# Performance work log

Measured on AMD Instinct MI355X. Metric: run time of the kernel, lower is better.

The kernel has to match this reference:

```python
import jax, jax.numpy as jnp
import numpy as np

B, S, H = 16, 4096, 1024


def setup_inputs() -> dict:
    key = jax.random.key(0)
    ks = jax.random.split(key, 8)
    scale = 1.0 / np.sqrt(H)
    return {
        "s_t_hat": jax.random.normal(ks[0], (B, H), jnp.float32),
        "encoder_outputs": jax.random.normal(ks[1], (B, S, H), jnp.float32),
        "encoder_feature": jax.random.normal(ks[2], (B * S, H), jnp.float32),
        "enc_padding_mask": jnp.ones((B, S), jnp.float32),
        "coverage": jax.random.uniform(ks[3], (B, S), jnp.float32),
        # params: decode_proj (Linear H->H with bias), W_c (Linear 1->H, no bias,
        # stored as an [H] column), v (Linear H->1, no bias, stored as [H])
        "W_dec": jax.random.normal(ks[4], (H, H), jnp.float32) * scale,
        "b_dec": jnp.zeros((H,), jnp.float32),
        "W_c": jax.random.normal(ks[5], (H,), jnp.float32),
        "v": jax.random.normal(ks[6], (H,), jnp.float32) * scale,
    }


def reference(s_t_hat, encoder_outputs, encoder_feature, enc_padding_mask,
              coverage, W_dec, b_dec, W_c, v):
    b, s, h = encoder_outputs.shape
    # decode_proj: [B, H]
    dec_fea = s_t_hat @ W_dec.T + b_dec
    # broadcast add over seq + coverage feature (Linear(1->H) == outer product)
    att = (encoder_feature.reshape(b, s, h)
           + dec_fea[:, None, :]
           + coverage[:, :, None] * W_c[None, None, :])
    e = jnp.tanh(att)
    scores = jnp.einsum('bsh,h->bs', e, v)
    # masked softmax with renormalization (is_word=True path)
    attn = jax.nn.softmax(scores, axis=1) * enc_padding_mask
    attn = attn / (attn.sum(axis=1, keepdims=True) + 1e-20)
    # context vector: weighted sum of encoder outputs
    c_t = jnp.einsum('bs,bsh->bh', attn, encoder_outputs)
    return c_t, attn, attn, scores
```

## Files before the change

kernel.cpp:

```cpp
#include <hip/hip_runtime.h>

#define BB 16
#define SS 4096
#define HH 1024
#define SSPLIT 64

__device__ __forceinline__ float fast_tanh(float x) {
    x = fminf(fmaxf(x, -15.0f), 15.0f);
    float e = __expf(-2.0f * x);
    return (1.0f - e) * __builtin_amdgcn_rcpf(1.0f + e);
}

__device__ __forceinline__ float wave_reduce_sum(float v) {
#pragma unroll
    for (int off = 32; off > 0; off >>= 1) v += __shfl_xor(v, off, 64);
    return v;
}

__global__ __launch_bounds__(256) void dec_fea_kernel(
    const float* __restrict__ s_t_hat, const float* __restrict__ W_dec,
    const float* __restrict__ b_dec, float* __restrict__ dec_fea)
{
    int wave = (blockIdx.x * blockDim.x + threadIdx.x) >> 6;
    int lane = threadIdx.x & 63;
    int b = wave >> 10;
    int h = wave & (HH - 1);
    const float4* st4 = (const float4*)(s_t_hat + (size_t)b * HH);
    const float4* wd4 = (const float4*)(W_dec + (size_t)h * HH);
    float acc = 0.0f;
#pragma unroll
    for (int j = 0; j < 4; ++j) {
        int idx = lane + 64 * j;
        float4 a = st4[idx];
        float4 w = wd4[idx];
        acc += a.x * w.x + a.y * w.y + a.z * w.z + a.w * w.w;
    }
    acc = wave_reduce_sum(acc);
    if (lane == 0) dec_fea[wave] = acc + b_dec[h];
}

__global__ __launch_bounds__(256) void scores_kernel(
    const float* __restrict__ ef, const float* __restrict__ dec_fea,
    const float* __restrict__ cov, const float* __restrict__ W_c,
    const float* __restrict__ v, float* __restrict__ scores)
{
    int row = (blockIdx.x * blockDim.x + threadIdx.x) >> 6;
    int lane = threadIdx.x & 63;
    int b = row >> 12;
    float cv = cov[row];
    const float4* ef4 = (const float4*)(ef + (size_t)row * HH);
    const float4* de4 = (const float4*)(dec_fea + (size_t)b * HH);
    const float4* wc4 = (const float4*)W_c;
    const float4* v4  = (const float4*)v;
    float acc = 0.0f;
#pragma unroll
    for (int j = 0; j < 4; ++j) {
        int idx = lane + 64 * j;
        float4 x  = ef4[idx];
        float4 d  = de4[idx];
        float4 w  = wc4[idx];
        float4 vv = v4[idx];
        acc += fast_tanh(x.x + d.x + cv * w.x) * vv.x;
        acc += fast_tanh(x.y + d.y + cv * w.y) * vv.y;
        acc += fast_tanh(x.z + d.z + cv * w.z) * vv.z;
        acc += fast_tanh(x.w + d.w + cv * w.w) * vv.w;
    }
    acc = wave_reduce_sum(acc);
    if (lane == 0) scores[row] = acc;
}

__global__ __launch_bounds__(1024) void softmax_kernel(
    const float* __restrict__ scores, const float* __restrict__ mask,
    float* __restrict__ attn1, float* __restrict__ attn2)
{
    int b = blockIdx.x;
    int tid = threadIdx.x;

    const float4* s4 = (const float4*)(scores + (size_t)b * SS);
    const float4* m4 = (const float4*)(mask + (size_t)b * SS);
    float4 sc = s4[tid];
    float4 mk = m4[tid];

    __shared__ float redA[16];
    __shared__ float redB[16];
    int wid = tid >> 6, lane = tid & 63;

    float mx = fmaxf(fmaxf(sc.x, sc.y), fmaxf(sc.z, sc.w));
#pragma unroll
    for (int off = 32; off > 0; off >>= 1) mx = fmaxf(mx, __shfl_xor(mx, off, 64));
    if (lane == 0) redA[wid] = mx;
    __syncthreads();
    float bm = redA[0];
#pragma unroll
    for (int i = 1; i < 16; ++i) bm = fmaxf(bm, redA[i]);
    __syncthreads();

    float4 e;
    e.x = __expf(sc.x - bm);
    e.y = __expf(sc.y - bm);
    e.z = __expf(sc.z - bm);
    e.w = __expf(sc.w - bm);
    float4 t;
    t.x = e.x * mk.x; t.y = e.y * mk.y; t.z = e.z * mk.z; t.w = e.w * mk.w;

    float se = wave_reduce_sum(e.x + e.y + e.z + e.w);
    float st = wave_reduce_sum(t.x + t.y + t.z + t.w);
    if (lane == 0) { redA[wid] = se; redB[wid] = st; }
    __syncthreads();
    float tot_e = 0.0f, tot_t = 0.0f;
#pragma unroll
    for (int i = 0; i < 16; ++i) { tot_e += redA[i]; tot_t += redB[i]; }

    float inv = 1.0f / tot_e;
    float r = 1.0f / (tot_t * inv + 1e-20f);
    float scale = inv * r;
    float4 a;
    a.x = t.x * scale; a.y = t.y * scale; a.z = t.z * scale; a.w = t.w * scale;
    ((float4*)(attn1 + (size_t)b * SS))[tid] = a;
    ((float4*)(attn2 + (size_t)b * SS))[tid] = a;
}

__global__ __launch_bounds__(256) void context_partial_kernel(
    const float* __restrict__ eo, const float* __restrict__ attn,
    float* __restrict__ partials)
{
    int b = blockIdx.y;
    int s0 = blockIdx.x * (SS / SSPLIT);
    int tid = threadIdx.x;
    const float4* eo4 = (const float4*)(eo + ((size_t)b * SS + s0) * HH);
    const float* at = attn + (size_t)b * SS + s0;
    float4 acc = {0.0f, 0.0f, 0.0f, 0.0f};
#pragma unroll 8
    for (int s = 0; s < SS / SSPLIT; ++s) {
        float a = at[s];
        float4 x = eo4[(size_t)s * 256 + tid];
        acc.x += a * x.x; acc.y += a * x.y; acc.z += a * x.z; acc.w += a * x.w;
    }
    float4* dst = (float4*)(partials + ((size_t)blockIdx.x * BB + b) * HH);
    dst[tid] = acc;
}

__global__ __launch_bounds__(256) void context_reduce_kernel(
    const float* __restrict__ partials, float* __restrict__ c_t)
{
    int gid = blockIdx.x * blockDim.x + threadIdx.x;
    const float4* p4 = (const float4*)partials;
    float4 acc = {0.0f, 0.0f, 0.0f, 0.0f};
#pragma unroll
    for (int s = 0; s < SSPLIT; ++s) {
        float4 x = p4[(size_t)s * (BB * HH / 4) + gid];
        acc.x += x.x; acc.y += x.y; acc.z += x.z; acc.w += x.w;
    }
    ((float4*)c_t)[gid] = acc;
}

extern "C" void kernel_launch(void* const* d_in, const int* in_sizes, int n_in,
                              void* d_out, int out_size, void* d_ws, size_t ws_size,
                              hipStream_t stream)
{
    const float* s_t_hat  = (const float*)d_in[0];
    const float* enc_out  = (const float*)d_in[1];
    const float* enc_feat = (const float*)d_in[2];
    const float* mask     = (const float*)d_in[3];
    const float* cov      = (const float*)d_in[4];
    const float* W_dec    = (const float*)d_in[5];
    const float* b_dec    = (const float*)d_in[6];
    const float* W_c      = (const float*)d_in[7];
    const float* v        = (const float*)d_in[8];

    float* out    = (float*)d_out;
    float* c_t    = out;
    float* attn1  = out + BB * HH;
    float* attn2  = attn1 + BB * SS;
    float* scores = attn2 + BB * SS;

    float* dec_fea  = (float*)d_ws;
    float* partials = dec_fea + BB * HH;

    dec_fea_kernel<<<dim3(BB * HH / 4), 256, 0, stream>>>(s_t_hat, W_dec, b_dec, dec_fea);
    scores_kernel<<<dim3(BB * SS / 4), 256, 0, stream>>>(enc_feat, dec_fea, cov, W_c, v, scores);
    softmax_kernel<<<dim3(BB), 1024, 0, stream>>>(scores, mask, attn1, attn2);
    context_partial_kernel<<<dim3(SSPLIT, BB), 256, 0, stream>>>(enc_out, attn1, partials);
    context_reduce_kernel<<<dim3(BB * HH / 1024), 256, 0, stream>>>(partials, c_t);
}
```

Measured before the change: 521.5 us.

## Fuse per-chunk softmax statistics into scores kernel and fold normalization into context

The scores kernel now processes 64-row chunks per block, keeps the dec_fea, W_c and v vectors in registers, and emits per-chunk online-softmax statistics (max, sum of exp, masked sum). A tiny merge kernel combines these per batch, and the context kernel recomputes the normalized attention weights from scores and writes attn directly. This removes the single-block-per-batch softmax kernel and shifts the per-row vector reloads into registers. The trade-off is a grid of only 1024 blocks in the scores kernel, where each wave works through 16 rows serially, so there is less parallelism than before.

```diff
diff --git a/kernel.cpp b/kernel.cpp
--- a/kernel.cpp
+++ b/kernel.cpp
@@ -3,7 +3,7 @@
 #define BB 16
 #define SS 4096
 #define HH 1024
-#define SSPLIT 64
+#define NCHUNK 64
 
 __device__ __forceinline__ float fast_tanh(float x) {
     x = fminf(fmaxf(x, -15.0f), 15.0f);
@@ -14,6 +14,12 @@
 __device__ __forceinline__ float wave_reduce_sum(float v) {
 #pragma unroll
     for (int off = 32; off > 0; off >>= 1) v += __shfl_xor(v, off, 64);
+    return v;
+}
+
+__device__ __forceinline__ float wave_reduce_max(float v) {
+#pragma unroll
+    for (int off = 32; off > 0; off >>= 1) v = fmaxf(v, __shfl_xor(v, off, 64));
     return v;
 }
 
@@ -39,119 +45,122 @@
     if (lane == 0) dec_fea[wave] = acc + b_dec[h];
 }
 
-__global__ __launch_bounds__(256) void scores_kernel(
+__global__ __launch_bounds__(256) void scores_stats_kernel(
     const float* __restrict__ ef, const float* __restrict__ dec_fea,
     const float* __restrict__ cov, const float* __restrict__ W_c,
-    const float* __restrict__ v, float* __restrict__ scores)
-{
-    int row = (blockIdx.x * blockDim.x + threadIdx.x) >> 6;
+    const float* __restrict__ v, const float* __restrict__ mask,
+    float* __restrict__ scores, float* __restrict__ stat_m,
+    float* __restrict__ stat_se, float* __restrict__ stat_st)
+{
+    int b = blockIdx.y;
+    int chunk = blockIdx.x;
+    int s0 = chunk * 64;
+    int wid = threadIdx.x >> 6;
     int lane = threadIdx.x & 63;
-    int b = row >> 12;
-    float cv = cov[row];
-    const float4* ef4 = (const float4*)(ef + (size_t)row * HH);
+    __shared__ float sc[64];
+
     const float4* de4 = (const float4*)(dec_fea + (size_t)b * HH);
     const float4* wc4 = (const float4*)W_c;
     const float4* v4  = (const float4*)v;
-    float acc = 0.0f;
+    float4 d[4], w[4], vv[4];
 #pragma unroll
     for (int j = 0; j < 4; ++j) {
         int idx = lane + 64 * j;
-        float4 x  = ef4[idx];
-        float4 d  = de4[idx];
-        float4 w  = wc4[idx];
-        float4 vv = v4[idx];
-        acc += fast_tanh(x.x + d.x + cv * w.x) * vv.x;
-        acc += fast_tanh(x.y + d.y + cv * w.y) * vv.y;
-        acc += fast_tanh(x.z + d.z + cv * w.z) * vv.z;
-        acc += fast_tanh(x.w + d.w + cv * w.w) * vv.w;
-    }
-    acc = wave_reduce_sum(acc);
-    if (lane == 0) scores[row] = acc;
-}
-
-__global__ __launch_bounds__(1024) void softmax_kernel(
-    const float* __restrict__ scores, const float* __restrict__ mask,
-    float* __restrict__ attn1, float* __restrict__ attn2)
-{
-    int b = blockIdx.x;
+        d[j] = de4[idx]; w[j] = wc4[idx]; vv[j] = v4[idx];
+    }
+
+    for (int r = 0; r < 16; ++r) {
+        int s = s0 + wid * 16 + r;
+        size_t row = (size_t)b * SS + s;
+        float cv = cov[row];
+        const float4* ef4 = (const float4*)(ef + row * HH);
+        float acc = 0.0f;
+#pragma unroll
+        for (int j = 0; j < 4; ++j) {
+            float4 x = ef4[lane + 64 * j];
+            acc += fast_tanh(x.x + d[j].x + cv * w[j].x) * vv[j].x;
+            acc += fast_tanh(x.y + d[j].y + cv * w[j].y) * vv[j].y;
+            acc += fast_tanh(x.z + d[j].z + cv * w[j].z) * vv[j].z;
+            acc += fast_tanh(x.w + d[j].w + cv * w[j].w) * vv[j].w;
+        }
+        acc = wave_reduce_sum(acc);
+        if (lane == 0) { sc[wid * 16 + r] = acc; scores[row] = acc; }
+    }
+    __syncthreads();
+
+    if (threadIdx.x < 64) {
+        float s_val = sc[lane];
+        float mk = mask[(size_t)b * SS + s0 + lane];
+        float m = wave_reduce_max(s_val);
+        float e = __expf(s_val - m);
+        float se = wave_reduce_sum(e);
+        float st = wave_reduce_sum(e * mk);
+        if (lane == 0) {
+            int idx = b * NCHUNK + chunk;
+            stat_m[idx] = m; stat_se[idx] = se; stat_st[idx] = st;
+        }
+    }
+}
+
+__global__ __launch_bounds__(1024) void stats_merge_kernel(
+    const float* __restrict__ stat_m, const float* __restrict__ stat_se,
+    const float* __restrict__ stat_st, float* __restrict__ Mb,
+    float* __restrict__ alpha_b)
+{
+    int b = threadIdx.x >> 6, lane = threadIdx.x & 63;
+    int idx = b * NCHUNK + lane;
+    float m = stat_m[idx], se = stat_se[idx], st = stat_st[idx];
+    float M = wave_reduce_max(m);
+    float scale = __expf(m - M);
+    float de = wave_reduce_sum(se * scale);
+    float dt = wave_reduce_sum(st * scale);
+    if (lane == 0) {
+        float inv = 1.0f / de;
+        alpha_b[b] = inv * (1.0f / (dt * inv + 1e-20f));
+        Mb[b] = M;
+    }
+}
+
+__global__ __launch_bounds__(256) void context_kernel(
+    const float* __restrict__ eo, const float* __restrict__ scores,
+    const float* __restrict__ mask, const float* __restrict__ Mb,
+    const float* __restrict__ alpha_b, float* __restrict__ attn1,
+    float* __restrict__ attn2, float* __restrict__ partials)
+{
+    int b = blockIdx.y, chunk = blockIdx.x, s0 = chunk * 64;
     int tid = threadIdx.x;
-
-    const float4* s4 = (const float4*)(scores + (size_t)b * SS);
-    const float4* m4 = (const float4*)(mask + (size_t)b * SS);
-    float4 sc = s4[tid];
-    float4 mk = m4[tid];
-
-    __shared__ float redA[16];
-    __shared__ float redB[16];
-    int wid = tid >> 6, lane = tid & 63;
-
-    float mx = fmaxf(fmaxf(sc.x, sc.y), fmaxf(sc.z, sc.w));
-#pragma unroll
-    for (int off = 32; off > 0; off >>= 1) mx = fmaxf(mx, __shfl_xor(mx, off, 64));
-    if (lane == 0) redA[wid] = mx;
+    __shared__ float wsh[64];
+    float M = Mb[b], a = alpha_b[b];
+    if (tid < 64) {
+        size_t s = (size_t)b * SS + s0 + tid;
+        float wv = __expf(scores[s] - M) * mask[s] * a;
+        wsh[tid] = wv;
+        attn1[s] = wv;
+        attn2[s] = wv;
+    }
     __syncthreads();
-    float bm = redA[0];
-#pragma unroll
-    for (int i = 1; i < 16; ++i) bm = fmaxf(bm, redA[i]);
-    __syncthreads();
-
-    float4 e;
-    e.x = __expf(sc.x - bm);
-    e.y = __expf(sc.y - bm);
-    e.z = __expf(sc.z - bm);
-    e.w = __expf(sc.w - bm);
-    float4 t;
-    t.x = e.x * mk.x; t.y = e.y * mk.y; t.z = e.z * mk.z; t.w = e.w * mk.w;
-
-    float se = wave_reduce_sum(e.x + e.y + e.z + e.w);
-    float st = wave_reduce_sum(t.x + t.y + t.z + t.w);
-    if (lane == 0) { redA[wid] = se; redB[wid] = st; }
-    __syncthreads();
-    float tot_e = 0.0f, tot_t = 0.0f;
-#pragma unroll
-    for (int i = 0; i < 16; ++i) { tot_e += redA[i]; tot_t += redB[i]; }
-
-    float inv = 1.0f / tot_e;
-    float r = 1.0f / (tot_t * inv + 1e-20f);
-    float scale = inv * r;
-    float4 a;
-    a.x = t.x * scale; a.y = t.y * scale; a.z = t.z * scale; a.w = t.w * scale;
-    ((float4*)(attn1 + (size_t)b * SS))[tid] = a;
-    ((float4*)(attn2 + (size_t)b * SS))[tid] = a;
-}
-
-__global__ __launch_bounds__(256) void context_partial_kernel(
-    const float* __restrict__ eo, const float* __restrict__ attn,
-    float* __restrict__ partials)
-{
-    int b = blockIdx.y;
-    int s0 = blockIdx.x * (SS / SSPLIT);
-    int tid = threadIdx.x;
     const float4* eo4 = (const float4*)(eo + ((size_t)b * SS + s0) * HH);
-    const float* at = attn + (size_t)b * SS + s0;
     float4 acc = {0.0f, 0.0f, 0.0f, 0.0f};
 #pragma unroll 8
-    for (int s = 0; s < SS / SSPLIT; ++s) {
-        float a = at[s];
+    for (int s = 0; s < 64; ++s) {
+        float wv = wsh[s];
         float4 x = eo4[(size_t)s * 256 + tid];
-        acc.x += a * x.x; acc.y += a * x.y; acc.z += a * x.z; acc.w += a * x.w;
-    }
-    float4* dst = (float4*)(partials + ((size_t)blockIdx.x * BB + b) * HH);
-    dst[tid] = acc;
+        acc.x += wv * x.x; acc.y += wv * x.y;
+        acc.z += wv * x.z; acc.w += wv * x.w;
+    }
+    ((float4*)(partials + ((size_t)chunk * BB + b) * HH))[tid] = acc;
 }
 
 __global__ __launch_bounds__(256) void context_reduce_kernel(
     const float* __restrict__ partials, float* __restrict__ c_t)
 {
-    int gid = blockIdx.x * blockDim.x + threadIdx.x;
-    const float4* p4 = (const float4*)partials;
-    float4 acc = {0.0f, 0.0f, 0.0f, 0.0f};
-#pragma unroll
-    for (int s = 0; s < SSPLIT; ++s) {
-        float4 x = p4[(size_t)s * (BB * HH / 4) + gid];
-        acc.x += x.x; acc.y += x.y; acc.z += x.z; acc.w += x.w;
-    }
-    ((float4*)c_t)[gid] = acc;
+    int b = blockIdx.x >> 2;
+    int h = (blockIdx.x & 3) * 256 + threadIdx.x;
+    float acc = 0.0f;
+#pragma unroll
+    for (int c = 0; c < NCHUNK; ++c)
+        acc += partials[((size_t)c * BB + b) * HH + h];
+    c_t[(size_t)b * HH + h] = acc;
 }
 
 extern "C" void kernel_launch(void* const* d_in, const int* in_sizes, int n_in,
@@ -176,10 +185,19 @@
 
     float* dec_fea  = (float*)d_ws;
     float* partials = dec_fea + BB * HH;
-
-    dec_fea_kernel<<<dim3(BB * HH / 4), 256, 0, stream>>>(s_t_hat, W_dec, b_dec, dec_fea);
-    scores_kernel<<<dim3(BB * SS / 4), 256, 0, stream>>>(enc_feat, dec_fea, cov, W_c, v, scores);
-    softmax_kernel<<<dim3(BB), 1024, 0, stream>>>(scores, mask, attn1, attn2);
-    context_partial_kernel<<<dim3(SSPLIT, BB), 256, 0, stream>>>(enc_out, attn1, partials);
-    context_reduce_kernel<<<dim3(BB * HH / 1024), 256, 0, stream>>>(partials, c_t);
-}
+    float* stat_m   = partials + NCHUNK * BB * HH;
+    float* stat_se  = stat_m + BB * NCHUNK;
+    float* stat_st  = stat_se + BB * NCHUNK;
+    float* Mb       = stat_st + BB * NCHUNK;
+    float* alpha_b  = Mb + BB;
+
+    dec_fea_kernel<<<dim3(BB * HH / 4), 256, 0, stream>>>(
+        s_t_hat, W_dec, b_dec, dec_fea);
+    scores_stats_kernel<<<dim3(NCHUNK, BB), 256, 0, stream>>>(
+        enc_feat, dec_fea, cov, W_c, v, mask, scores, stat_m, stat_se, stat_st);
+    stats_merge_kernel<<<dim3(1), 1024, 0, stream>>>(
+        stat_m, stat_se, stat_st, Mb, alpha_b);
+    context_kernel<<<dim3(NCHUNK, BB), 256, 0, stream>>>(
+        enc_out, scores, mask, Mb, alpha_b, attn1, attn2, partials);
+    context_reduce_kernel<<<dim3(64), 256, 0, stream>>>(partials, c_t);
+}
```

After: 544.0 us. 1.04x slower.
